# Kernel optimization log

Hardware: AMD Instinct MI355X
Metric: run time of the kernel (lower is better)

The kernel has to match this reference:

```python
import jax, jax.numpy as jnp
import numpy as np
from jax import lax

B, S, F, D, H, L, A = 16, 512, 64, 512, 8, 4, 3
E = D // H  # head_dim = 64

def _gelu(t):
    return jax.nn.gelu(t, approximate=False)  # torch nn.GELU() is exact erf

def _make_masks():
    i = jnp.arange(S)[:, None]
    j = jnp.arange(S)[None, :]
    d = jnp.abs(i - j)
    ms = []
    for h in range(min(5, H)):
        dil = 2 ** h
        ms.append((d <= dil) | (d % (2 ** (h + 1)) == 0))
    m = jnp.stack(ms)  # [5,S,S] bool
    idx = jnp.minimum(jnp.arange(H), m.shape[0] - 1)
    return m[idx]  # [H,S,S]

MASKS = _make_masks()

def _ln(x, g, b, eps=1e-5):
    mu = jnp.mean(x, -1, keepdims=True)
    var = jnp.mean((x - mu) ** 2, -1, keepdims=True)
    return (x - mu) * lax.rsqrt(var + eps) * g + b

def _conv1d(x_ncw, w, b):
    y = lax.conv_general_dilated(x_ncw, w, (1,), [(1, 1)],
                                 dimension_numbers=("NCH", "OIH", "NCH"))
    return y + b[None, :, None]

def _attn(x, Wq, bq, Wk, bk, Wv, bv, Wo, bo):
    # x: [B,S,D]; Wq/Wk/Wv: [H,E,D] (stacked per-head Linear weights)
    q = jnp.einsum("bsd,hed->bhse", x, Wq) + bq[None, :, None, :]
    k = jnp.einsum("bsd,hed->bhse", x, Wk) + bk[None, :, None, :]
    v = jnp.einsum("bsd,hed->bhse", x, Wv) + bv[None, :, None, :]
    s = jnp.einsum("bhse,bhte->bhst", q, k) / (E ** 0.5)
    s = jnp.where(MASKS[None], s, -jnp.inf)  # log-sparse masked_fill
    p = jax.nn.softmax(s, axis=-1)
    o = jnp.einsum("bhst,bhte->bhse", p, v)
    o = o.transpose(0, 2, 1, 3).reshape(x.shape[0], x.shape[1], D)  # concat heads
    return o @ Wo.T + bo

def _forward(x, conv1_w, conv1_b, conv2_w, conv2_b, emb_w, emb_b, pos,
             Wq, bq, Wk, bk, Wv, bv, Wo, bo, ln1_g, ln1_b, ln2_g, ln2_b,
             W1, b1, W2, b2, lnf_g, lnf_b,
             a1_w, a1_b, a2_w, a2_b, a3_w, a3_b, a4_w, a4_b,
             c1_w, c1_b, c2_w, c2_b, c3_w, c3_b, c4_w, c4_b):
    # feature extractor: two conv1d+GELU over time axis
    h0 = _gelu(_conv1d(x.transpose(0, 2, 1), conv1_w, conv1_b))
    h0 = _gelu(_conv1d(h0, conv2_w, conv2_b)).transpose(0, 2, 1)  # [B,S,D]
    z = h0 @ emb_w.T + emb_b + pos[:, :S]  # input embedding + positional
    for l in range(L):  # PyraFormer blocks (pre-norm residual)
        z = z + _attn(_ln(z, ln1_g[l], ln1_b[l]),
                      Wq[l], bq[l], Wk[l], bk[l], Wv[l], bv[l], Wo[l], bo[l])
        h = _ln(z, ln2_g[l], ln2_b[l])
        z = z + (_gelu(h @ W1[l].T + b1[l]) @ W2[l].T + b2[l])
    z = _ln(z, lnf_g, lnf_b)
    feat = z[:, -1, :]  # last timestep features

    def head(f, layers):
        (w1, bb1), (w2, bb2), (w3, bb3), (w4, bb4) = layers
        f = _gelu(f @ w1.T + bb1)
        f = _gelu(f @ w2.T + bb2)
        f = _gelu(f @ w3.T + bb3)
        return f @ w4.T + bb4

    policy = head(feat, [(a1_w, a1_b), (a2_w, a2_b), (a3_w, a3_b), (a4_w, a4_b)])
    value = head(feat, [(c1_w, c1_b), (c2_w, c2_b), (c3_w, c3_b), (c4_w, c4_b)])
    return policy, value

def setup_inputs() -> dict:
    key = jax.random.key(0)
    ks = iter(jax.random.split(key, 64))
    r = lambda shape, s=0.05: jax.random.normal(next(ks), shape, jnp.float32) * s
    return {
        "x": jax.random.normal(next(ks), (B, S, F), jnp.float32),
        "conv1_w": r((D // 2, F, 3)), "conv1_b": jnp.zeros((D // 2,)),
        "conv2_w": r((D, D // 2, 3)), "conv2_b": jnp.zeros((D,)),
        "emb_w": r((D, D)), "emb_b": jnp.zeros((D,)),
        "pos": r((1, S, D), 0.02),
        "Wq": r((L, H, E, D)), "bq": jnp.zeros((L, H, E)),
        "Wk": r((L, H, E, D)), "bk": jnp.zeros((L, H, E)),
        "Wv": r((L, H, E, D)), "bv": jnp.zeros((L, H, E)),
        "Wo": r((L, D, D)), "bo": jnp.zeros((L, D)),
        "ln1_g": jnp.ones((L, D)), "ln1_b": jnp.zeros((L, D)),
        "ln2_g": jnp.ones((L, D)), "ln2_b": jnp.zeros((L, D)),
        "W1": r((L, 4 * D, D)), "b1": jnp.zeros((L, 4 * D)),
        "W2": r((L, D, 4 * D)), "b2": jnp.zeros((L, D)),
        "lnf_g": jnp.ones((D,)), "lnf_b": jnp.zeros((D,)),
        "a1_w": r((128, D)), "a1_b": jnp.zeros((128,)),
        "a2_w": r((256, 128)), "a2_b": jnp.zeros((256,)),
        "a3_w": r((57, 256)), "a3_b": jnp.zeros((57,)),
        "a4_w": r((A, 57)), "a4_b": jnp.zeros((A,)),
        "c1_w": r((128, D)), "c1_b": jnp.zeros((128,)),
        "c2_w": r((256, 128)), "c2_b": jnp.zeros((256,)),
        "c3_w": r((57, 256)), "c3_b": jnp.zeros((57,)),
        "c4_w": r((1, 57)), "c4_b": jnp.zeros((1,)),
    }

def reference(x, conv1_w, conv1_b, conv2_w, conv2_b, emb_w, emb_b, pos,
              Wq, bq, Wk, bk, Wv, bv, Wo, bo, ln1_g, ln1_b, ln2_g, ln2_b,
              W1, b1, W2, b2, lnf_g, lnf_b,
              a1_w, a1_b, a2_w, a2_b, a3_w, a3_b, a4_w, a4_b,
              c1_w, c1_b, c2_w, c2_b, c3_w, c3_b, c4_w, c4_b):
    return _forward(x, conv1_w, conv1_b, conv2_w, conv2_b, emb_w, emb_b, pos,
                    Wq, bq, Wk, bk, Wv, bv, Wo, bo, ln1_g, ln1_b, ln2_g, ln2_b,
                    W1, b1, W2, b2, lnf_g, lnf_b,
                    a1_w, a1_b, a2_w, a2_b, a3_w, a3_b, a4_w, a4_b,
                    c1_w, c1_b, c2_w, c2_b, c3_w, c3_b, c4_w, c4_b)
```

## Files before the change

kernel.cpp:

```cpp
#include <hip/hip_runtime.h>
#include <hip/hip_bf16.h>
#include <cstdint>

typedef __attribute__((ext_vector_type(8))) short bf16x8;
typedef __attribute__((ext_vector_type(4))) float f32x4;
typedef unsigned short u16;

#define DEV __device__ __forceinline__

DEV float b2f(u16 u) {
  union { unsigned int i; float f; } v; v.i = ((unsigned int)u) << 16; return v.f;
}
DEV u16 f2b(float f) {
  __hip_bfloat16 h = __float2bfloat16(f);
  return *reinterpret_cast<u16*>(&h);
}
DEV float erf_fast(float x) {
  float ax = fabsf(x);
  float t = __builtin_amdgcn_rcpf(fmaf(0.3275911f, ax, 1.0f));
  float p = t * fmaf(t, fmaf(t, fmaf(t, fmaf(t, 1.061405429f, -1.453152027f),
                                     1.421413741f), -0.284496736f), 0.254829592f);
  float r = fmaf(-p, __expf(-ax * ax), 1.0f);
  return copysignf(r, x);
}
DEV float gelu_f(float x) { return 0.5f * x * (1.0f + erf_fast(x * 0.70710678118654752f)); }

DEV void async_cp16(const u16* g, u16* l) {
  __builtin_amdgcn_global_load_lds(
      (const __attribute__((address_space(1))) void*)g,
      (__attribute__((address_space(3))) void*)l, 16, 0, 0);
}

__global__ void probe_kernel(const unsigned int* __restrict__ g, int* __restrict__ flag) {
  if (threadIdx.x == 0 && blockIdx.x == 0) *flag = (*g == 0x3F800000u) ? 1 : 0;
}

struct CvtArgs {
  const void* src[42];
  unsigned int off[43];
};

struct alignas(16) U8v { u16 u[8]; };
struct alignas(8)  U4v { u16 u[4]; };

__global__ __launch_bounds__(256) void cvt_kernel(CvtArgs a, int n_t, unsigned int total,
                                                  const int* __restrict__ flag,
                                                  u16* __restrict__ dst) {
  unsigned int i8 = (blockIdx.x * 256u + threadIdx.x) * 8u;
  if (i8 >= total) return;
  int t = 0;
  while (t + 1 < n_t && i8 >= a.off[t + 1]) t++;
  unsigned int j = i8 - a.off[t];
  bool in_seg = (i8 + 8 <= a.off[t + 1]) && (i8 + 8 <= total);
  int fp32 = *flag;
  if (fp32) {
    if (in_seg && ((j & 3) == 0)) {
      const float* s = (const float*)a.src[t] + j;
      float4 v0 = *(const float4*)s;
      float4 v1 = *(const float4*)(s + 4);
      U8v o;
      o.u[0] = f2b(v0.x); o.u[1] = f2b(v0.y); o.u[2] = f2b(v0.z); o.u[3] = f2b(v0.w);
      o.u[4] = f2b(v1.x); o.u[5] = f2b(v1.y); o.u[6] = f2b(v1.z); o.u[7] = f2b(v1.w);
      *(U8v*)(dst + i8) = o;
    } else {
      for (int k = 0; k < 8; k++) {
        unsigned int i = i8 + k;
        if (i >= total) break;
        int tt = t;
        while (tt + 1 < n_t && i >= a.off[tt + 1]) tt++;
        dst[i] = f2b(((const float*)a.src[tt])[i - a.off[tt]]);
      }
    }
  } else {
    if (in_seg && ((j & 7) == 0)) {
      *(U8v*)(dst + i8) = *(const U8v*)((const u16*)a.src[t] + j);
    } else {
      for (int k = 0; k < 8; k++) {
        unsigned int i = i8 + k;
        if (i >= total) break;
        int tt = t;
        while (tt + 1 < n_t && i >= a.off[tt + 1]) tt++;
        dst[i] = ((const u16*)a.src[tt])[i - a.off[tt]];
      }
    }
  }
}

__global__ __launch_bounds__(256) void gemm_bt(
    const u16* __restrict__ A, const u16* __restrict__ W,
    const u16* __restrict__ bias,
    u16* __restrict__ outB, float* __restrict__ outF,
    int N, int K, int kLen, int mode)
{
  __shared__ __align__(16) u16 As[2][128 * 32];
  __shared__ __align__(16) u16 Bs[2][128 * 32];
  int t = threadIdx.x, l = t & 63, w = t >> 6;
  int wr = w >> 1, wc = w & 1;
  int col = l & 15, quad = l >> 4;
  int q8 = (quad ^ ((col >> 1) & 3)) * 8;
  int m0 = blockIdx.x * 128;
  int n0 = blockIdx.y * 128;
  int k0 = blockIdx.z * kLen;

  f32x4 acc[4][4];
#pragma unroll
  for (int i = 0; i < 4; i++)
#pragma unroll
    for (int j = 0; j < 4; j++) acc[i][j] = (f32x4){0.f, 0.f, 0.f, 0.f};

  int g1i = t, g2i = t + 256;
  int r1 = g1i >> 2, r2 = g2i >> 2;
  int cb1 = (g1i & 3) ^ ((r1 >> 1) & 3);
  int cb2 = (g2i & 3) ^ ((r2 >> 1) & 3);
  const u16* a1 = A + (size_t)(m0 + r1) * K + k0 + cb1 * 8;
  const u16* a2 = A + (size_t)(m0 + r2) * K + k0 + cb2 * 8;
  const u16* b1 = W + (size_t)(n0 + r1) * K + k0 + cb1 * 8;
  const u16* b2 = W + (size_t)(n0 + r2) * K + k0 + cb2 * 8;

  int nK = kLen >> 5;
  async_cp16(a1, &As[0][g1i * 8]);
  async_cp16(a2, &As[0][g2i * 8]);
  async_cp16(b1, &Bs[0][g1i * 8]);
  async_cp16(b2, &Bs[0][g2i * 8]);
  for (int ki = 0; ki < nK; ki++) {
    int cur = ki & 1;
    if (ki + 1 < nK) {
      int nxt = cur ^ 1, kt = (ki + 1) << 5;
      async_cp16(a1 + kt, &As[nxt][g1i * 8]);
      async_cp16(a2 + kt, &As[nxt][g2i * 8]);
      async_cp16(b1 + kt, &Bs[nxt][g1i * 8]);
      async_cp16(b2 + kt, &Bs[nxt][g2i * 8]);
      __builtin_amdgcn_s_waitcnt(0x0F74);
    } else {
      __builtin_amdgcn_s_waitcnt(0x0F70);
    }
    __builtin_amdgcn_s_barrier();
    __builtin_amdgcn_sched_barrier(0);
    bf16x8 af[4], bfv[4];
#pragma unroll
    for (int mi = 0; mi < 4; mi++)
      af[mi] = *(const bf16x8*)&As[cur][(wr * 64 + mi * 16 + col) * 32 + q8];
#pragma unroll
    for (int ni = 0; ni < 4; ni++)
      bfv[ni] = *(const bf16x8*)&Bs[cur][(wc * 64 + ni * 16 + col) * 32 + q8];
#pragma unroll
    for (int mi = 0; mi < 4; mi++)
#pragma unroll
      for (int ni = 0; ni < 4; ni++)
        acc[mi][ni] = __builtin_amdgcn_mfma_f32_16x16x32_bf16(bfv[ni], af[mi], acc[mi][ni], 0, 0, 0);
    __builtin_amdgcn_sched_barrier(0);
    __builtin_amdgcn_s_barrier();
  }

  int mBase = m0 + wr * 64, nBase = n0 + wc * 64;
  if (mode == 1) {
#pragma unroll
    for (int mi = 0; mi < 4; mi++) {
      int m = mBase + mi * 16 + col;
      size_t rowOff = (size_t)m * N;
#pragma unroll
      for (int ni = 0; ni < 4; ni++) {
        int n4 = nBase + ni * 16 + quad * 4;
        U4v bb = *(const U4v*)&bias[n4];
        f32x4 v = acc[mi][ni];
        U4v o;
#pragma unroll
        for (int r = 0; r < 4; r++) o.u[r] = f2b(gelu_f(v[r] + b2f(bb.u[r])));
        *(U4v*)&outB[rowOff + n4] = o;
      }
    }
  } else {
#pragma unroll
    for (int mi = 0; mi < 4; mi++) {
      int m = mBase + mi * 16 + col;
      size_t rowOff = (size_t)m * N;
#pragma unroll
      for (int ni = 0; ni < 4; ni++) {
        int n4 = nBase + ni * 16 + quad * 4;
        U4v bb = *(const U4v*)&bias[n4];
        f32x4 v = acc[mi][ni];
        float4* p = (float4*)&outF[rowOff + n4];
        float4 zv = *p;
        zv.x += v[0] + b2f(bb.u[0]);
        zv.y += v[1] + b2f(bb.u[1]);
        zv.z += v[2] + b2f(bb.u[2]);
        zv.w += v[3] + b2f(bb.u[3]);
        *p = zv;
      }
    }
  }
}

__global__ __launch_bounds__(256) void gemm_bt64(
    const u16* __restrict__ A, const u16* __restrict__ W,
    const u16* __restrict__ bias,
    u16* __restrict__ outB, float* __restrict__ outF,
    int N, int K, int mode)
{
  __shared__ __align__(16) u16 As[2][64 * 32];
  __shared__ __align__(16) u16 Bs[2][128 * 32];
  int t = threadIdx.x, l = t & 63, w = t >> 6;
  int wr = w >> 1, wc = w & 1;
  int col = l & 15, quad = l >> 4;
  int q8 = (quad ^ ((col >> 1) & 3)) * 8;
  int m0 = blockIdx.x * 64;
  int n0 = blockIdx.y * 128;

  f32x4 acc[2][4];
#pragma unroll
  for (int i = 0; i < 2; i++)
#pragma unroll
    for (int j = 0; j < 4; j++) acc[i][j] = (f32x4){0.f, 0.f, 0.f, 0.f};

  int ra = t >> 2;
  int ca = (t & 3) ^ ((ra >> 1) & 3);
  int g1i = t, g2i = t + 256;
  int rb1 = g1i >> 2, rb2 = g2i >> 2;
  int cb1 = (g1i & 3) ^ ((rb1 >> 1) & 3);
  int cb2 = (g2i & 3) ^ ((rb2 >> 1) & 3);
  const u16* a1 = A + (size_t)(m0 + ra) * K + ca * 8;
  const u16* b1 = W + (size_t)(n0 + rb1) * K + cb1 * 8;
  const u16* b2 = W + (size_t)(n0 + rb2) * K + cb2 * 8;

  int nK = K >> 5;
  async_cp16(a1, &As[0][t * 8]);
  async_cp16(b1, &Bs[0][g1i * 8]);
  async_cp16(b2, &Bs[0][g2i * 8]);
  for (int ki = 0; ki < nK; ki++) {
    int cur = ki & 1;
    if (ki + 1 < nK) {
      int nxt = cur ^ 1, kt = (ki + 1) << 5;
      async_cp16(a1 + kt, &As[nxt][t * 8]);
      async_cp16(b1 + kt, &Bs[nxt][g1i * 8]);
      async_cp16(b2 + kt, &Bs[nxt][g2i * 8]);
      __builtin_amdgcn_s_waitcnt(0x0F73);
    } else {
      __builtin_amdgcn_s_waitcnt(0x0F70);
    }
    __builtin_amdgcn_s_barrier();
    __builtin_amdgcn_sched_barrier(0);
    bf16x8 af[2], bfv[4];
#pragma unroll
    for (int mi = 0; mi < 2; mi++)
      af[mi] = *(const bf16x8*)&As[cur][(wr * 32 + mi * 16 + col) * 32 + q8];
#pragma unroll
    for (int ni = 0; ni < 4; ni++)
      bfv[ni] = *(const bf16x8*)&Bs[cur][(wc * 64 + ni * 16 + col) * 32 + q8];
#pragma unroll
    for (int mi = 0; mi < 2; mi++)
#pragma unroll
      for (int ni = 0; ni < 4; ni++)
        acc[mi][ni] = __builtin_amdgcn_mfma_f32_16x16x32_bf16(bfv[ni], af[mi], acc[mi][ni], 0, 0, 0);
    __builtin_amdgcn_sched_barrier(0);
    __builtin_amdgcn_s_barrier();
  }

  int mBase = m0 + wr * 32, nBase = n0 + wc * 64;
  if (mode == 1) {
#pragma unroll
    for (int mi = 0; mi < 2; mi++) {
      int m = mBase + mi * 16 + col;
      size_t rowOff = (size_t)m * N;
#pragma unroll
      for (int ni = 0; ni < 4; ni++) {
        int n4 = nBase + ni * 16 + quad * 4;
        U4v bb = *(const U4v*)&bias[n4];
        f32x4 v = acc[mi][ni];
        U4v o;
#pragma unroll
        for (int r = 0; r < 4; r++) o.u[r] = f2b(gelu_f(v[r] + b2f(bb.u[r])));
        *(U4v*)&outB[rowOff + n4] = o;
      }
    }
  } else {
#pragma unroll
    for (int mi = 0; mi < 2; mi++) {
      int m = mBase + mi * 16 + col;
      size_t rowOff = (size_t)m * N;
#pragma unroll
      for (int ni = 0; ni < 4; ni++) {
        int n4 = nBase + ni * 16 + quad * 4;
        U4v bb = *(const U4v*)&bias[n4];
        f32x4 v = acc[mi][ni];
        float4* p = (float4*)&outF[rowOff + n4];
        float4 zv = *p;
        zv.x += v[0] + b2f(bb.u[0]);
        zv.y += v[1] + b2f(bb.u[1]);
        zv.z += v[2] + b2f(bb.u[2]);
        zv.w += v[3] + b2f(bb.u[3]);
        *p = zv;
      }
    }
  }
}

__global__ __launch_bounds__(256) void gemm_qkv(
    const u16* __restrict__ A,
    const u16* __restrict__ Wq, const u16* __restrict__ Wk, const u16* __restrict__ Wv,
    const u16* __restrict__ bq, const u16* __restrict__ bk, const u16* __restrict__ bv,
    u16* __restrict__ outQ, u16* __restrict__ outK, u16* __restrict__ outVT, int K)
{
  __shared__ __align__(16) u16 As[2][128 * 32];
  __shared__ __align__(16) u16 Bs[2][128 * 32];
  int t = threadIdx.x, l = t & 63, w = t >> 6;
  int wr = w >> 1, wc = w & 1;
  int col = l & 15, quad = l >> 4;
  int q8 = (quad ^ ((col >> 1) & 3)) * 8;
  int m0 = blockIdx.x * 128;
  int sel = blockIdx.y >> 2;
  int n0 = (blockIdx.y & 3) * 128;
  const u16* W = sel == 0 ? Wq : (sel == 1 ? Wk : Wv);
  const u16* bias = sel == 0 ? bq : (sel == 1 ? bk : bv);
  const bool swp = (sel < 2);

  f32x4 acc[4][4];
#pragma unroll
  for (int i = 0; i < 4; i++)
#pragma unroll
    for (int j = 0; j < 4; j++) acc[i][j] = (f32x4){0.f, 0.f, 0.f, 0.f};

  int g1i = t, g2i = t + 256;
  int r1 = g1i >> 2, r2 = g2i >> 2;
  int cb1 = (g1i & 3) ^ ((r1 >> 1) & 3);
  int cb2 = (g2i & 3) ^ ((r2 >> 1) & 3);
  const u16* a1 = A + (size_t)(m0 + r1) * K + cb1 * 8;
  const u16* a2 = A + (size_t)(m0 + r2) * K + cb2 * 8;
  const u16* b1 = W + (size_t)(n0 + r1) * K + cb1 * 8;
  const u16* b2 = W + (size_t)(n0 + r2) * K + cb2 * 8;

  int nK = K >> 5;
  async_cp16(a1, &As[0][g1i * 8]);
  async_cp16(a2, &As[0][g2i * 8]);
  async_cp16(b1, &Bs[0][g1i * 8]);
  async_cp16(b2, &Bs[0][g2i * 8]);
  for (int ki = 0; ki < nK; ki++) {
    int cur = ki & 1;
    if (ki + 1 < nK) {
      int nxt = cur ^ 1, kt = (ki + 1) << 5;
      async_cp16(a1 + kt, &As[nxt][g1i * 8]);
      async_cp16(a2 + kt, &As[nxt][g2i * 8]);
      async_cp16(b1 + kt, &Bs[nxt][g1i * 8]);
      async_cp16(b2 + kt, &Bs[nxt][g2i * 8]);
      __builtin_amdgcn_s_waitcnt(0x0F74);
    } else {
      __builtin_amdgcn_s_waitcnt(0x0F70);
    }
    __builtin_amdgcn_s_barrier();
    __builtin_amdgcn_sched_barrier(0);
    bf16x8 af[4], bfv[4];
#pragma unroll
    for (int mi = 0; mi < 4; mi++)
      af[mi] = *(const bf16x8*)&As[cur][(wr * 64 + mi * 16 + col) * 32 + q8];
#pragma unroll
    for (int ni = 0; ni < 4; ni++)
      bfv[ni] = *(const bf16x8*)&Bs[cur][(wc * 64 + ni * 16 + col) * 32 + q8];
    if (swp) {
#pragma unroll
      for (int mi = 0; mi < 4; mi++)
#pragma unroll
        for (int ni = 0; ni < 4; ni++)
          acc[mi][ni] = __builtin_amdgcn_mfma_f32_16x16x32_bf16(bfv[ni], af[mi], acc[mi][ni], 0, 0, 0);
    } else {
#pragma unroll
      for (int mi = 0; mi < 4; mi++)
#pragma unroll
        for (int ni = 0; ni < 4; ni++)
          acc[mi][ni] = __builtin_amdgcn_mfma_f32_16x16x32_bf16(af[mi], bfv[ni], acc[mi][ni], 0, 0, 0);
    }
    __builtin_amdgcn_sched_barrier(0);
    __builtin_amdgcn_s_barrier();
  }

  int mBase = m0 + wr * 64, nBase = n0 + wc * 64;
  if (swp) {
    u16* outB = sel == 0 ? outQ : outK;
#pragma unroll
    for (int mi = 0; mi < 4; mi++) {
      int m = mBase + mi * 16 + col;
      size_t rowOff = (size_t)m * 512;
#pragma unroll
      for (int ni = 0; ni < 4; ni++) {
        int n4 = nBase + ni * 16 + quad * 4;
        U4v bb = *(const U4v*)&bias[n4];
        f32x4 v = acc[mi][ni];
        U4v o;
#pragma unroll
        for (int r = 0; r < 4; r++) o.u[r] = f2b(v[r] + b2f(bb.u[r]));
        *(U4v*)&outB[rowOff + n4] = o;
      }
    }
  } else {
    int b = m0 >> 9;
    int sB = m0 & 511;
#pragma unroll
    for (int mi = 0; mi < 4; mi++) {
      int s4 = sB + wr * 64 + mi * 16 + quad * 4;
#pragma unroll
      for (int ni = 0; ni < 4; ni++) {
        int n = nBase + ni * 16 + col;
        int h = n >> 6, e = n & 63;
        float bvv = b2f(bias[n]);
        f32x4 v = acc[mi][ni];
        U4v o;
#pragma unroll
        for (int r = 0; r < 4; r++) o.u[r] = f2b(v[r] + bvv);
        *(U4v*)&outVT[((size_t)((b * 8 + h) * 64 + e)) * 512 + s4] = o;
      }
    }
  }
}

__global__ __launch_bounds__(256) void zinit_kernel(const u16* __restrict__ pos,
                                                    float* __restrict__ z)
{
  int i = (blockIdx.x * 256 + threadIdx.x) * 8;
  int n = i & 511;
  int m = i >> 9;
  int s = m & 511;
  U8v p = *(const U8v*)&pos[s * 512 + n];
  float4 o0 = {b2f(p.u[0]), b2f(p.u[1]), b2f(p.u[2]), b2f(p.u[3])};
  float4 o1 = {b2f(p.u[4]), b2f(p.u[5]), b2f(p.u[6]), b2f(p.u[7])};
  *(float4*)(z + i) = o0;
  *(float4*)(z + i + 4) = o1;
}

__global__ void im2col3_kernel(const u16* __restrict__ src,
                               u16* __restrict__ dst, int C)
{
  int m = blockIdx.x;
  int k = blockIdx.y * blockDim.x + threadIdx.x;
  int ci = k / 3;
  int tap = k - ci * 3;
  int s = m & 511;
  int sp = s + tap - 1;
  u16 val = 0;
  if (sp >= 0 && sp < 512) val = src[(size_t)(m + tap - 1) * C + ci];
  dst[(size_t)m * (3 * C) + k] = val;
}

__global__ __launch_bounds__(256) void ln_kernel(
    const float* __restrict__ z, const u16* __restrict__ gam,
    const u16* __restrict__ bet, u16* __restrict__ out)
{
  int w = threadIdx.x >> 6, l = threadIdx.x & 63;
  int row = blockIdx.x * 4 + w;
  const float* zr = z + (size_t)row * 512;
  float4 v0 = *(const float4*)(zr + l * 8);
  float4 v1 = *(const float4*)(zr + l * 8 + 4);
  float x[8] = {v0.x, v0.y, v0.z, v0.w, v1.x, v1.y, v1.z, v1.w};
  float s = 0.f;
#pragma unroll
  for (int i = 0; i < 8; i++) s += x[i];
#pragma unroll
  for (int mm = 1; mm < 64; mm <<= 1) s += __shfl_xor(s, mm, 64);
  float mu = s * (1.0f / 512.0f);
  float vs = 0.f;
#pragma unroll
  for (int i = 0; i < 8; i++) { float d = x[i] - mu; vs += d * d; }
#pragma unroll
  for (int mm = 1; mm < 64; mm <<= 1) vs += __shfl_xor(vs, mm, 64);
  float rs = rsqrtf(vs * (1.0f / 512.0f) + 1e-5f);
  U8v gg = *(const U8v*)(gam + l * 8);
  U8v bb = *(const U8v*)(bet + l * 8);
  U8v o;
#pragma unroll
  for (int i = 0; i < 8; i++) o.u[i] = f2b((x[i] - mu) * rs * b2f(gg.u[i]) + b2f(bb.u[i]));
  *(U8v*)(out + (size_t)row * 512 + l * 8) = o;
}

__global__ __launch_bounds__(256) void lnf_kernel(
    const float* __restrict__ z, const u16* __restrict__ gam,
    const u16* __restrict__ bet, u16* __restrict__ feat)
{
  int w = threadIdx.x >> 6, l = threadIdx.x & 63;
  int b = blockIdx.x * 4 + w;
  const float* zr = z + ((size_t)b * 512 + 511) * 512;
  float4 v0 = *(const float4*)(zr + l * 8);
  float4 v1 = *(const float4*)(zr + l * 8 + 4);
  float x[8] = {v0.x, v0.y, v0.z, v0.w, v1.x, v1.y, v1.z, v1.w};
  float s = 0.f;
#pragma unroll
  for (int i = 0; i < 8; i++) s += x[i];
#pragma unroll
  for (int mm = 1; mm < 64; mm <<= 1) s += __shfl_xor(s, mm, 64);
  float mu = s * (1.0f / 512.0f);
  float vs = 0.f;
#pragma unroll
  for (int i = 0; i < 8; i++) { float d = x[i] - mu; vs += d * d; }
#pragma unroll
  for (int mm = 1; mm < 64; mm <<= 1) vs += __shfl_xor(vs, mm, 64);
  float rs = rsqrtf(vs * (1.0f / 512.0f) + 1e-5f);
  U8v gg = *(const U8v*)(gam + l * 8);
  U8v bb = *(const U8v*)(bet + l * 8);
  U8v o;
#pragma unroll
  for (int i = 0; i < 8; i++) o.u[i] = f2b((x[i] - mu) * rs * b2f(gg.u[i]) + b2f(bb.u[i]));
  *(U8v*)(feat + (size_t)b * 512 + l * 8) = o;
}

#define AST 72
__global__ __launch_bounds__(256) void attn_kernel(
    const u16* __restrict__ Q, const u16* __restrict__ Kg,
    const u16* __restrict__ VT, u16* __restrict__ O)
{
  __shared__ __align__(16) u16 Qs[64 * AST];
  __shared__ __align__(16) u16 Ks[64 * AST];
  __shared__ __align__(16) u16 Vts[64 * AST];
  __shared__ __align__(16) u16 Ps[64 * AST];
  const float NEG = -1e30f;
  int bh = blockIdx.y; int b = bh >> 3, h = bh & 7;
  int i0 = blockIdx.x * 64;
  int t = threadIdx.x, w = t >> 6, l = t & 63;
  int col = l & 15, quad = l >> 4;
  int dil = 1 << (h < 4 ? h : 4);
  int per_m1 = 2 * dil - 1;

  {
    int row = t >> 2, c = (t & 3) * 16;
    const u16* src = Q + ((size_t)(b * 512 + i0 + row) * 512 + h * 64 + c);
    *(float4*)&Qs[row * AST + c] = *(const float4*)src;
    *(float4*)&Qs[row * AST + c + 8] = *(const float4*)(src + 8);
  }
  __syncthreads();

  bf16x8 qa[2];
#pragma unroll
  for (int kk = 0; kk < 2; kk++)
    qa[kk] = *(const bf16x8*)&Qs[(w * 16 + col) * AST + kk * 32 + quad * 8];

  f32x4 acc_o[4];
#pragma unroll
  for (int i = 0; i < 4; i++) acc_o[i] = (f32x4){0.f, 0.f, 0.f, 0.f};
  float m_run[4], l_run[4];
#pragma unroll
  for (int r = 0; r < 4; r++) { m_run[r] = NEG; l_run[r] = 0.f; }

  for (int jt = 0; jt < 8; jt++) {
    int j0 = jt * 64;
    {
      int row = t >> 2, c = (t & 3) * 16;
      const u16* ks = Kg + ((size_t)(b * 512 + j0 + row) * 512 + h * 64 + c);
      *(float4*)&Ks[row * AST + c] = *(const float4*)ks;
      *(float4*)&Ks[row * AST + c + 8] = *(const float4*)(ks + 8);
      const u16* vs = VT + ((size_t)(bh * 64 + row) * 512 + j0 + c);
      *(float4*)&Vts[row * AST + c] = *(const float4*)vs;
      *(float4*)&Vts[row * AST + c + 8] = *(const float4*)(vs + 8);
    }
    __syncthreads();

    f32x4 sa[4];
#pragma unroll
    for (int ni = 0; ni < 4; ni++) {
      f32x4 s = (f32x4){0.f, 0.f, 0.f, 0.f};
#pragma unroll
      for (int kk = 0; kk < 2; kk++) {
        bf16x8 kb = *(const bf16x8*)&Ks[(ni * 16 + col) * AST + kk * 32 + quad * 8];
        s = __builtin_amdgcn_mfma_f32_16x16x32_bf16(qa[kk], kb, s, 0, 0, 0);
      }
      sa[ni] = s;
    }

    float pv[4][4];
    float alpha_r[4];
#pragma unroll
    for (int r = 0; r < 4; r++) {
      int ig = i0 + w * 16 + quad * 4 + r;
      float sv[4]; float mx = NEG;
#pragma unroll
      for (int ni = 0; ni < 4; ni++) {
        int jg = j0 + ni * 16 + col;
        int d = ig - jg; d = d < 0 ? -d : d;
        bool keep = (d <= dil) || ((d & per_m1) == 0);
        float s = keep ? fminf(sa[ni][r] * 0.125f, 80.0f) : NEG;
        sv[ni] = s; mx = fmaxf(mx, s);
      }
#pragma unroll
      for (int mm = 1; mm < 16; mm <<= 1) mx = fmaxf(mx, __shfl_xor(mx, mm, 64));
      float mN = fmaxf(m_run[r], mx);
      float a = __expf(m_run[r] - mN);
      float rsum = 0.f;
#pragma unroll
      for (int ni = 0; ni < 4; ni++) { float p = __expf(sv[ni] - mN); pv[ni][r] = p; rsum += p; }
#pragma unroll
      for (int mm = 1; mm < 16; mm <<= 1) rsum += __shfl_xor(rsum, mm, 64);
      l_run[r] = l_run[r] * a + rsum;
      m_run[r] = mN;
      alpha_r[r] = a;
    }
#pragma unroll
    for (int ne = 0; ne < 4; ne++)
#pragma unroll
      for (int r = 0; r < 4; r++) acc_o[ne][r] *= alpha_r[r];
#pragma unroll
    for (int ni = 0; ni < 4; ni++)
#pragma unroll
      for (int r = 0; r < 4; r++)
        Ps[(w * 16 + quad * 4 + r) * AST + ni * 16 + col] = f2b(pv[ni][r]);
    __syncthreads();

    bf16x8 pa[2];
#pragma unroll
    for (int kk = 0; kk < 2; kk++)
      pa[kk] = *(const bf16x8*)&Ps[(w * 16 + col) * AST + kk * 32 + quad * 8];
#pragma unroll
    for (int ne = 0; ne < 4; ne++) {
#pragma unroll
      for (int kk = 0; kk < 2; kk++) {
        bf16x8 vb = *(const bf16x8*)&Vts[(ne * 16 + col) * AST + kk * 32 + quad * 8];
        acc_o[ne] = __builtin_amdgcn_mfma_f32_16x16x32_bf16(pa[kk], vb, acc_o[ne], 0, 0, 0);
      }
    }
    __syncthreads();
  }

  float inv[4];
#pragma unroll
  for (int r = 0; r < 4; r++) inv[r] = 1.0f / fmaxf(l_run[r], 1e-20f);
#pragma unroll
  for (int ne = 0; ne < 4; ne++)
#pragma unroll
    for (int r = 0; r < 4; r++) {
      float o = acc_o[ne][r] * inv[r];
      O[((size_t)(b * 512 + i0 + w * 16 + quad * 4 + r)) * 512 + h * 64 + ne * 16 + col] = f2b(o);
    }
}

__global__ __launch_bounds__(256) void heads_kernel(
    const u16* __restrict__ feat,
    const u16* __restrict__ a1w, const u16* __restrict__ a1b,
    const u16* __restrict__ a2w, const u16* __restrict__ a2b,
    const u16* __restrict__ a3w, const u16* __restrict__ a3b,
    const u16* __restrict__ a4w, const u16* __restrict__ a4b,
    const u16* __restrict__ c1w, const u16* __restrict__ c1b,
    const u16* __restrict__ c2w, const u16* __restrict__ c2b,
    const u16* __restrict__ c3w, const u16* __restrict__ c3b,
    const u16* __restrict__ c4w, const u16* __restrict__ c4b,
    const int* __restrict__ flag, void* __restrict__ outv)
{
  __shared__ float f[512];
  __shared__ float g1[256];
  __shared__ float g2[512];
  __shared__ float g3[128];
  int b = blockIdx.x, t = threadIdx.x;
  f[t] = b2f(feat[b * 512 + t]);
  f[t + 256] = b2f(feat[b * 512 + 256 + t]);
  __syncthreads();
  {
    const u16* wrow; float bias;
    if (t < 128) { wrow = a1w + (size_t)t * 512; bias = b2f(a1b[t]); }
    else { wrow = c1w + (size_t)(t - 128) * 512; bias = b2f(c1b[t - 128]); }
    float s = bias;
    for (int k = 0; k < 512; k++) s += b2f(wrow[k]) * f[k];
    g1[t] = gelu_f(s);
  }
  __syncthreads();
  {
    float s1 = b2f(a2b[t]);
    for (int k = 0; k < 128; k++) s1 += b2f(a2w[t * 128 + k]) * g1[k];
    float s2 = b2f(c2b[t]);
    for (int k = 0; k < 128; k++) s2 += b2f(c2w[t * 128 + k]) * g1[128 + k];
    g2[t] = gelu_f(s1);
    g2[256 + t] = gelu_f(s2);
  }
  __syncthreads();
  if (t < 57) {
    float s = b2f(a3b[t]);
    for (int k = 0; k < 256; k++) s += b2f(a3w[t * 256 + k]) * g2[k];
    g3[t] = gelu_f(s);
  } else if (t >= 64 && t < 121) {
    int u = t - 64;
    float s = b2f(c3b[u]);
    for (int k = 0; k < 256; k++) s += b2f(c3w[u * 256 + k]) * g2[256 + k];
    g3[64 + u] = gelu_f(s);
  }
  __syncthreads();
  int fp32out = *flag;
  if (t < 3) {
    float s = b2f(a4b[t]);
    for (int k = 0; k < 57; k++) s += b2f(a4w[t * 57 + k]) * g3[k];
    if (fp32out) ((float*)outv)[b * 3 + t] = s;
    else ((u16*)outv)[b * 3 + t] = f2b(s);
  } else if (t == 4) {
    float s = b2f(c4b[0]);
    for (int k = 0; k < 57; k++) s += b2f(c4w[k]) * g3[64 + k];
    if (fp32out) ((float*)outv)[48 + b] = s;
    else ((u16*)outv)[48 + b] = f2b(s);
  }
}

extern "C" void kernel_launch(void* const* d_in, const int* in_sizes, int n_in,
                              void* d_out, int out_size, void* d_ws, size_t ws_size,
                              hipStream_t stream)
{
  char* ws = (char*)d_ws;
  float* z    = (float*)ws;
  u16* R      = (u16*)(ws + (16u << 20));
  u16* bufQ   = R;
  u16* bufK   = (u16*)(ws + (24u << 20));
  u16* bufO   = (u16*)(ws + (32u << 20));
  u16* bufVT  = (u16*)(ws + (40u << 20));
  u16* bufH   = (u16*)(ws + (48u << 20));
  u16* feat   = R;
  u16* pool   = (u16*)(ws + (56u << 20));
  int* flag   = (int*)(ws + (88u << 20));

  CvtArgs args;
  unsigned int off = 0;
  int nt = n_in < 42 ? n_in : 42;
  for (int i = 0; i < nt; i++) { args.src[i] = d_in[i]; args.off[i] = off; off += (unsigned int)in_sizes[i]; }
  args.off[nt] = off;
  unsigned int total = off;

  probe_kernel<<<1, 64, 0, stream>>>((const unsigned int*)d_in[24], flag);
  cvt_kernel<<<(total + 2047) / 2048, 256, 0, stream>>>(args, nt, total, flag, pool);

  const u16* P[42];
  for (int i = 0; i < nt; i++) P[i] = pool + args.off[i];
  const u16* x       = P[0];
  const u16* conv1_w = P[1];  const u16* conv1_b = P[2];
  const u16* conv2_w = P[3];  const u16* conv2_b = P[4];
  const u16* emb_w   = P[5];  const u16* emb_b   = P[6];
  const u16* pos     = P[7];
  const u16* Wq      = P[8];  const u16* bq      = P[9];
  const u16* Wk      = P[10]; const u16* bk      = P[11];
  const u16* Wv      = P[12]; const u16* bv      = P[13];
  const u16* Wo      = P[14]; const u16* bo      = P[15];
  const u16* ln1_g   = P[16]; const u16* ln1_b   = P[17];
  const u16* ln2_g   = P[18]; const u16* ln2_b   = P[19];
  const u16* W1      = P[20]; const u16* b1      = P[21];
  const u16* W2      = P[22]; const u16* b2      = P[23];
  const u16* lnf_g   = P[24]; const u16* lnf_b   = P[25];

  im2col3_kernel<<<dim3(8192, 1), 192, 0, stream>>>(x, R, 64);
  gemm_bt64<<<dim3(128, 2), 256, 0, stream>>>(R, conv1_w, conv1_b, bufH, nullptr, 256, 192, 1);
  im2col3_kernel<<<dim3(8192, 3), 256, 0, stream>>>(bufH, R, 256);
  gemm_bt64<<<dim3(128, 4), 256, 0, stream>>>(R, conv2_w, conv2_b, bufH, nullptr, 512, 768, 1);
  zinit_kernel<<<2048, 256, 0, stream>>>(pos, z);
  gemm_bt64<<<dim3(128, 4), 256, 0, stream>>>(bufH, emb_w, emb_b, nullptr, z, 512, 512, 2);

  for (int l = 0; l < 4; l++) {
    ln_kernel<<<2048, 256, 0, stream>>>(z, ln1_g + l * 512, ln1_b + l * 512, bufH);
    gemm_qkv<<<dim3(64, 12), 256, 0, stream>>>(bufH,
        Wq + (size_t)l * 262144, Wk + (size_t)l * 262144, Wv + (size_t)l * 262144,
        bq + l * 512, bk + l * 512, bv + l * 512, bufQ, bufK, bufVT, 512);
    attn_kernel<<<dim3(8, 128), 256, 0, stream>>>(bufQ, bufK, bufVT, bufO);
    gemm_bt64<<<dim3(128, 4), 256, 0, stream>>>(bufO, Wo + (size_t)l * 262144, bo + l * 512, nullptr, z, 512, 512, 2);
    ln_kernel<<<2048, 256, 0, stream>>>(z, ln2_g + l * 512, ln2_b + l * 512, bufH);
    gemm_bt<<<dim3(64, 16, 1), 256, 0, stream>>>(bufH, W1 + (size_t)l * 1048576, b1 + l * 2048, R, nullptr, 2048, 512, 512, 1);
    gemm_bt64<<<dim3(128, 4), 256, 0, stream>>>(R, W2 + (size_t)l * 1048576, b2 + l * 512, nullptr, z, 512, 2048, 2);
  }

  lnf_kernel<<<4, 256, 0, stream>>>(z, lnf_g, lnf_b, feat);
  heads_kernel<<<16, 256, 0, stream>>>(feat,
      P[26], P[27], P[28], P[29], P[30], P[31], P[32], P[33],
      P[34], P[35], P[36], P[37], P[38], P[39], P[40], P[41],
      flag, d_out);
}
```

Baseline: 969.5 us.

## Transpose attention scores, fold softmax scale into Q, drop Q smem and barriers

Folds the 1/sqrt(E) scale into the Q projection epilogue and computes S^T via swapped MFMA operands, so each lane owns one query row and softmax needs only two cross-lane shuffles instead of per-row 16-lane reductions. Q staging reuses the P buffer and the block barriers around Q and P are replaced with waitcnt, since each wave only touches its own rows. Adds s_setprio around the MFMA sections and flattens the grid so consecutive blocks cover different heads. It also drops the score clamp at 80 and relies on wave-local LDS ordering for correctness, which is a risk.

Result: faster. 927.2 us (-4.4%).

```diff
diff --git a/kernel.cpp b/kernel.cpp
--- a/kernel.cpp
+++ b/kernel.cpp
@@ -312,6 +312,7 @@
   const u16* W = sel == 0 ? Wq : (sel == 1 ? Wk : Wv);
   const u16* bias = sel == 0 ? bq : (sel == 1 ? bk : bv);
   const bool swp = (sel < 2);
+  const float scl = sel == 0 ? 0.125f : 1.0f;
 
   f32x4 acc[4][4];
 #pragma unroll
@@ -385,7 +386,7 @@
         f32x4 v = acc[mi][ni];
         U4v o;
 #pragma unroll
-        for (int r = 0; r < 4; r++) o.u[r] = f2b(v[r] + b2f(bb.u[r]));
+        for (int r = 0; r < 4; r++) o.u[r] = f2b((v[r] + b2f(bb.u[r])) * scl);
         *(U4v*)&outB[rowOff + n4] = o;
       }
     }
@@ -503,13 +504,14 @@
     const u16* __restrict__ Q, const u16* __restrict__ Kg,
     const u16* __restrict__ VT, u16* __restrict__ O)
 {
-  __shared__ __align__(16) u16 Qs[64 * AST];
   __shared__ __align__(16) u16 Ks[64 * AST];
   __shared__ __align__(16) u16 Vts[64 * AST];
   __shared__ __align__(16) u16 Ps[64 * AST];
   const float NEG = -1e30f;
-  int bh = blockIdx.y; int b = bh >> 3, h = bh & 7;
-  int i0 = blockIdx.x * 64;
+  int blk = blockIdx.x;
+  int bh = blk & 127;
+  int i0 = (blk >> 7) * 64;
+  int b = bh >> 3, h = bh & 7;
   int t = threadIdx.x, w = t >> 6, l = t & 63;
   int col = l & 15, quad = l >> 4;
   int dil = 1 << (h < 4 ? h : 4);
@@ -518,22 +520,21 @@
   {
     int row = t >> 2, c = (t & 3) * 16;
     const u16* src = Q + ((size_t)(b * 512 + i0 + row) * 512 + h * 64 + c);
-    *(float4*)&Qs[row * AST + c] = *(const float4*)src;
-    *(float4*)&Qs[row * AST + c + 8] = *(const float4*)(src + 8);
-  }
-  __syncthreads();
-
+    *(float4*)&Ps[row * AST + c] = *(const float4*)src;
+    *(float4*)&Ps[row * AST + c + 8] = *(const float4*)(src + 8);
+  }
+  __builtin_amdgcn_s_waitcnt(0xC07F);
+  __builtin_amdgcn_sched_barrier(0);
   bf16x8 qa[2];
 #pragma unroll
   for (int kk = 0; kk < 2; kk++)
-    qa[kk] = *(const bf16x8*)&Qs[(w * 16 + col) * AST + kk * 32 + quad * 8];
+    qa[kk] = *(const bf16x8*)&Ps[(w * 16 + col) * AST + kk * 32 + quad * 8];
 
   f32x4 acc_o[4];
 #pragma unroll
   for (int i = 0; i < 4; i++) acc_o[i] = (f32x4){0.f, 0.f, 0.f, 0.f};
-  float m_run[4], l_run[4];
-#pragma unroll
-  for (int r = 0; r < 4; r++) { m_run[r] = NEG; l_run[r] = 0.f; }
+  float m_run = NEG, l_run = 0.f;
+  int ig = i0 + w * 16 + col;
 
   for (int jt = 0; jt < 8; jt++) {
     int j0 = jt * 64;
@@ -549,59 +550,72 @@
     __syncthreads();
 
     f32x4 sa[4];
+    __builtin_amdgcn_s_setprio(1);
 #pragma unroll
     for (int ni = 0; ni < 4; ni++) {
       f32x4 s = (f32x4){0.f, 0.f, 0.f, 0.f};
 #pragma unroll
       for (int kk = 0; kk < 2; kk++) {
         bf16x8 kb = *(const bf16x8*)&Ks[(ni * 16 + col) * AST + kk * 32 + quad * 8];
-        s = __builtin_amdgcn_mfma_f32_16x16x32_bf16(qa[kk], kb, s, 0, 0, 0);
+        s = __builtin_amdgcn_mfma_f32_16x16x32_bf16(kb, qa[kk], s, 0, 0, 0);
       }
       sa[ni] = s;
     }
-
-    float pv[4][4];
-    float alpha_r[4];
-#pragma unroll
-    for (int r = 0; r < 4; r++) {
-      int ig = i0 + w * 16 + quad * 4 + r;
-      float sv[4]; float mx = NEG;
-#pragma unroll
-      for (int ni = 0; ni < 4; ni++) {
-        int jg = j0 + ni * 16 + col;
+    __builtin_amdgcn_s_setprio(0);
+
+    float mx = NEG;
+#pragma unroll
+    for (int ni = 0; ni < 4; ni++)
+#pragma unroll
+      for (int r = 0; r < 4; r++) {
+        int jg = j0 + ni * 16 + quad * 4 + r;
         int d = ig - jg; d = d < 0 ? -d : d;
         bool keep = (d <= dil) || ((d & per_m1) == 0);
-        float s = keep ? fminf(sa[ni][r] * 0.125f, 80.0f) : NEG;
-        sv[ni] = s; mx = fmaxf(mx, s);
-      }
-#pragma unroll
-      for (int mm = 1; mm < 16; mm <<= 1) mx = fmaxf(mx, __shfl_xor(mx, mm, 64));
-      float mN = fmaxf(m_run[r], mx);
-      float a = __expf(m_run[r] - mN);
-      float rsum = 0.f;
-#pragma unroll
-      for (int ni = 0; ni < 4; ni++) { float p = __expf(sv[ni] - mN); pv[ni][r] = p; rsum += p; }
-#pragma unroll
-      for (int mm = 1; mm < 16; mm <<= 1) rsum += __shfl_xor(rsum, mm, 64);
-      l_run[r] = l_run[r] * a + rsum;
-      m_run[r] = mN;
-      alpha_r[r] = a;
-    }
+        float s = keep ? sa[ni][r] : NEG;
+        sa[ni][r] = s;
+        mx = fmaxf(mx, s);
+      }
+    mx = fmaxf(mx, __shfl_xor(mx, 16, 64));
+    mx = fmaxf(mx, __shfl_xor(mx, 32, 64));
+    float mN = fmaxf(m_run, mx);
+    float alpha = __expf(m_run - mN);
+    m_run = mN;
+    float rsum = 0.f;
+#pragma unroll
+    for (int ni = 0; ni < 4; ni++)
+#pragma unroll
+      for (int r = 0; r < 4; r++) {
+        float p = __expf(sa[ni][r] - mN);
+        sa[ni][r] = p;
+        rsum += p;
+      }
+    rsum += __shfl_xor(rsum, 16, 64);
+    rsum += __shfl_xor(rsum, 32, 64);
+    l_run = l_run * alpha + rsum;
+
+#pragma unroll
+    for (int ni = 0; ni < 4; ni++) {
+      unsigned int lo = (unsigned int)f2b(sa[ni][0]) | ((unsigned int)f2b(sa[ni][1]) << 16);
+      unsigned int hi = (unsigned int)f2b(sa[ni][2]) | ((unsigned int)f2b(sa[ni][3]) << 16);
+      uint2 pk; pk.x = lo; pk.y = hi;
+      *(uint2*)&Ps[(w * 16 + col) * AST + ni * 16 + quad * 4] = pk;
+    }
+    __builtin_amdgcn_s_waitcnt(0xC07F);
+    __builtin_amdgcn_sched_barrier(0);
+
+    float a_sh[4];
+#pragma unroll
+    for (int r = 0; r < 4; r++) a_sh[r] = __shfl(alpha, quad * 4 + r, 64);
 #pragma unroll
     for (int ne = 0; ne < 4; ne++)
 #pragma unroll
-      for (int r = 0; r < 4; r++) acc_o[ne][r] *= alpha_r[r];
-#pragma unroll
-    for (int ni = 0; ni < 4; ni++)
-#pragma unroll
-      for (int r = 0; r < 4; r++)
-        Ps[(w * 16 + quad * 4 + r) * AST + ni * 16 + col] = f2b(pv[ni][r]);
-    __syncthreads();
+      for (int r = 0; r < 4; r++) acc_o[ne][r] *= a_sh[r];
 
     bf16x8 pa[2];
 #pragma unroll
     for (int kk = 0; kk < 2; kk++)
       pa[kk] = *(const bf16x8*)&Ps[(w * 16 + col) * AST + kk * 32 + quad * 8];
+    __builtin_amdgcn_s_setprio(1);
 #pragma unroll
     for (int ne = 0; ne < 4; ne++) {
 #pragma unroll
@@ -610,12 +624,16 @@
         acc_o[ne] = __builtin_amdgcn_mfma_f32_16x16x32_bf16(pa[kk], vb, acc_o[ne], 0, 0, 0);
       }
     }
+    __builtin_amdgcn_s_setprio(0);
     __syncthreads();
   }
 
   float inv[4];
 #pragma unroll
-  for (int r = 0; r < 4; r++) inv[r] = 1.0f / fmaxf(l_run[r], 1e-20f);
+  for (int r = 0; r < 4; r++) {
+    float lr = __shfl(l_run, quad * 4 + r, 64);
+    inv[r] = 1.0f / fmaxf(lr, 1e-20f);
+  }
 #pragma unroll
   for (int ne = 0; ne < 4; ne++)
 #pragma unroll
@@ -743,7 +761,7 @@
     gemm_qkv<<<dim3(64, 12), 256, 0, stream>>>(bufH,
         Wq + (size_t)l * 262144, Wk + (size_t)l * 262144, Wv + (size_t)l * 262144,
         bq + l * 512, bk + l * 512, bv + l * 512, bufQ, bufK, bufVT, 512);
-    attn_kernel<<<dim3(8, 128), 256, 0, stream>>>(bufQ, bufK, bufVT, bufO);
+    attn_kernel<<<dim3(1024), 256, 0, stream>>>(bufQ, bufK, bufVT, bufO);
     gemm_bt64<<<dim3(128, 4), 256, 0, stream>>>(bufO, Wo + (size_t)l * 262144, bo + l * 512, nullptr, z, 512, 512, 2);
     ln_kernel<<<2048, 256, 0, stream>>>(z, ln2_g + l * 512, ln2_b + l * 512, bufH);
     gemm_bt<<<dim3(64, 16, 1), 256, 0, stream>>>(bufH, W1 + (size_t)l * 1048576, b1 + l * 2048, R, nullptr, 2048, 512, 512, 1);
```
